# Performance work log

Measured on AMD Instinct MI355X. Metric: run time of the kernel, lower is better.

Reference implementation:

```python
import jax, jax.numpy as jnp
import numpy as np

D_MODEL = 1024
N_HEADS = 16
HEAD_DIM = D_MODEL // N_HEADS
B, S = 4, 2048


def setup_inputs() -> dict:
    key = jax.random.key(0)
    ks = jax.random.split(key, 12)
    s = 0.02
    q_input = jax.random.normal(ks[0], (B, S, D_MODEL), jnp.float32)
    k_input = jax.random.normal(ks[1], (B, S, D_MODEL), jnp.float32)
    v_input = jax.random.normal(ks[2], (B, S, D_MODEL), jnp.float32)
    # tail padding: keys at position >= valid_len are masked (True = pad)
    valid_len = jax.random.randint(ks[3], (B, 1), S // 2, S + 1)
    key_padding_mask = jnp.arange(S)[None, :] >= valid_len  # [B, S] bool
    Wq = jax.random.normal(ks[4], (D_MODEL, D_MODEL), jnp.float32) * s
    Wk = jax.random.normal(ks[5], (D_MODEL, D_MODEL), jnp.float32) * s
    Wv = jax.random.normal(ks[6], (D_MODEL, D_MODEL), jnp.float32) * s
    Wo = jax.random.normal(ks[7], (D_MODEL, D_MODEL), jnp.float32) * s
    bq = jnp.zeros((D_MODEL,), jnp.float32)
    bk = jnp.zeros((D_MODEL,), jnp.float32)
    bv = jnp.zeros((D_MODEL,), jnp.float32)
    bo = jnp.zeros((D_MODEL,), jnp.float32)
    return dict(q_input=q_input, k_input=k_input, v_input=v_input,
                key_padding_mask=key_padding_mask,
                Wq=Wq, bq=bq, Wk=Wk, bk=bk, Wv=Wv, bv=bv, Wo=Wo, bo=bo)


def reference(q_input, k_input, v_input, key_padding_mask, Wq, bq, Wk, bk, Wv, bv, Wo, bo):
    b, sq, d = q_input.shape
    sk = k_input.shape[1]
    Q = q_input @ Wq + bq
    K = k_input @ Wk + bk
    V = v_input @ Wv + bv
    # [B, H, S, Dh]
    Qh = Q.reshape(b, sq, N_HEADS, HEAD_DIM).transpose(0, 2, 1, 3)
    Kh = K.reshape(b, sk, N_HEADS, HEAD_DIM).transpose(0, 2, 1, 3)
    Vh = V.reshape(b, sk, N_HEADS, HEAD_DIM).transpose(0, 2, 1, 3)
    scores = jnp.einsum('bhqd,bhkd->bhqk', Qh, Kh) / jnp.sqrt(jnp.float32(HEAD_DIM))
    # causal mask (use_mask=True): triu(ones, diagonal=1)
    causal = jnp.triu(jnp.ones((sq, sk), bool), k=1)[None, None]
    scores = jnp.where(causal, -jnp.inf, scores)
    # key padding mask [B,1,1,Sk]
    scores = jnp.where(key_padding_mask[:, None, None, :], -jnp.inf, scores)
    all_inf = jnp.all(jnp.isinf(scores))
    probs = jax.nn.softmax(scores, axis=-1)
    probs = jnp.where(all_inf, jnp.float32(1.0) / sk, probs)
    # dropout(p=0.1) is identity in eval mode
    out = jnp.einsum('bhqk,bhkd->bhqd', probs, Vh)
    out = out.transpose(0, 2, 1, 3).reshape(b, sq, d)
    return out @ Wo + bo
```

## Files before the change

### kernel.cpp

```cpp
#include <hip/hip_runtime.h>

typedef unsigned short u16;
typedef unsigned int u32;
typedef u16 u16x8 __attribute__((ext_vector_type(8)));
typedef u16 u16x4v __attribute__((ext_vector_type(4)));
typedef u32 u32x2 __attribute__((ext_vector_type(2)));
typedef u32 u32x4 __attribute__((ext_vector_type(4)));
typedef __bf16 bf16x8 __attribute__((ext_vector_type(8)));
typedef float f32x4 __attribute__((ext_vector_type(4)));
typedef float f32x16 __attribute__((ext_vector_type(16)));

__device__ __forceinline__ u16 f2bf(float f) {
  unsigned u = __builtin_bit_cast(unsigned, f);
  u += 0x7FFF + ((u >> 16) & 1);
  return (u16)(u >> 16);
}

__device__ __forceinline__ float fast_exp2(float x) {
  return __builtin_amdgcn_exp2f(x);
}

__device__ __forceinline__ f32x4 mfma16(u16x8 a, u16x8 b, f32x4 c) {
  return __builtin_amdgcn_mfma_f32_16x16x32_bf16(
      __builtin_bit_cast(bf16x8, a), __builtin_bit_cast(bf16x8, b), c, 0, 0, 0);
}

__device__ __forceinline__ f32x16 mfma32(u16x8 a, u16x8 b, f32x16 c) {
  return __builtin_amdgcn_mfma_f32_32x32x16_bf16(
      __builtin_bit_cast(bf16x8, a), __builtin_bit_cast(bf16x8, b), c, 0, 0, 0);
}

__device__ __forceinline__ u32 cvt_pk_bf16(float lo, float hi) {
  u32 r;
  asm("v_cvt_pk_bf16_f32 %0, %1, %2" : "=v"(r) : "v"(lo), "v"(hi));
  return r;
}

constexpr int DM   = 1024;
constexpr int GK   = 1024;
constexpr int SEQ  = 2048;
constexpr int NB   = 4;
constexpr int NH   = 16;
constexpr int BK   = 64;
constexpr int LSTR = 72;

__global__ void transpose_cast_kernel(const float* __restrict__ W, u16* __restrict__ Wt) {
  __shared__ float tile[32][33];
  const int tx = threadIdx.x;
  const int ty = threadIdx.y;
  const int n0 = blockIdx.x * 32;
  const int k0 = blockIdx.y * 32;
#pragma unroll
  for (int i = 0; i < 4; ++i)
    tile[ty + i * 8][tx] = W[(size_t)(k0 + ty + i * 8) * DM + n0 + tx];
  __syncthreads();
#pragma unroll
  for (int i = 0; i < 4; ++i)
    Wt[(size_t)(n0 + ty + i * 8) * DM + k0 + tx] = f2bf(tile[tx][ty + i * 8]);
}

__global__ void vlen_kernel(const int* __restrict__ mask, int* __restrict__ vlen) {
  const int b = blockIdx.x;
  const int t = threadIdx.x;
  __shared__ int cnt[256];
  int c = 0;
  for (int s = t; s < SEQ; s += 256) c += (mask[b * SEQ + s] == 0) ? 1 : 0;
  cnt[t] = c;
  __syncthreads();
  for (int off = 128; off > 0; off >>= 1) {
    if (t < off) cnt[t] += cnt[t + off];
    __syncthreads();
  }
  if (t == 0) vlen[b] = cnt[0];
}

template <bool A_FP32>
__global__ __launch_bounds__(256) void gemm_kernel(const void* __restrict__ Av,
                                                   const u16* __restrict__ Bt,
                                                   const float* __restrict__ bias,
                                                   void* __restrict__ outv,
                                                   int out_mode) {
  __shared__ __align__(16) u16 lds_a[128 * LSTR];
  __shared__ __align__(16) u16 lds_b[128 * LSTR];
  const int tid  = threadIdx.x;
  const int lane = tid & 63;
  const int w    = tid >> 6;
  const int wm   = (w >> 1) * 64;
  const int wn   = (w & 1) * 64;
  const int lrow = lane & 15;
  const int lk   = (lane >> 4) * 8;
  const int n0   = blockIdx.x * 128;
  const int m0   = blockIdx.y * 128;

  f32x4 acc[4][4] = {};

  for (int kt = 0; kt < GK; kt += BK) {
    __syncthreads();
    if (A_FP32) {
      const float* A = (const float*)Av;
#pragma unroll
      for (int i = 0; i < 8; ++i) {
        int idx = tid + i * 256;
        int row = idx >> 4, q = idx & 15;
        float4 v = *(const float4*)(A + (size_t)(m0 + row) * GK + kt + q * 4);
        u16x4v hv = {f2bf(v.x), f2bf(v.y), f2bf(v.z), f2bf(v.w)};
        *(u16x4v*)(&lds_a[row * LSTR + q * 4]) = hv;
      }
    } else {
      const u16* A = (const u16*)Av;
#pragma unroll
      for (int i = 0; i < 4; ++i) {
        int idx = tid + i * 256;
        int row = idx >> 3, q = idx & 7;
        *(u16x8*)(&lds_a[row * LSTR + q * 8]) =
            *(const u16x8*)(A + (size_t)(m0 + row) * GK + kt + q * 8);
      }
    }
#pragma unroll
    for (int i = 0; i < 4; ++i) {
      int idx = tid + i * 256;
      int row = idx >> 3, q = idx & 7;
      *(u16x8*)(&lds_b[row * LSTR + q * 8]) =
          *(const u16x8*)(Bt + (size_t)(n0 + row) * GK + kt + q * 8);
    }
    __syncthreads();
#pragma unroll
    for (int kk = 0; kk < BK; kk += 32) {
      u16x8 am[4], bn[4];
#pragma unroll
      for (int m = 0; m < 4; ++m)
        am[m] = *(const u16x8*)(&lds_a[(wm + m * 16 + lrow) * LSTR + kk + lk]);
#pragma unroll
      for (int n = 0; n < 4; ++n)
        bn[n] = *(const u16x8*)(&lds_b[(wn + n * 16 + lrow) * LSTR + kk + lk]);
#pragma unroll
      for (int m = 0; m < 4; ++m)
#pragma unroll
        for (int n = 0; n < 4; ++n)
          acc[m][n] = mfma16(am[m], bn[n], acc[m][n]);
    }
  }

  const int r0 = (lane >> 4) * 4;
#pragma unroll
  for (int m = 0; m < 4; ++m) {
#pragma unroll
    for (int n = 0; n < 4; ++n) {
      const int col = n0 + wn + n * 16 + lrow;
      const float bval = bias[col];
#pragma unroll
      for (int r = 0; r < 4; ++r) {
        const int row = m0 + wm + m * 16 + r0 + r;
        const float v = acc[m][n][r] + bval;
        if (out_mode == 2) {
          ((float*)outv)[(size_t)row * DM + col] = v;
        } else {
          const int bb = row >> 11, s = row & (SEQ - 1);
          const int h = col >> 6, d = col & 63;
          size_t off;
          if (out_mode == 0) off = (((size_t)(bb * NH + h)) * SEQ + s) * 64 + d;
          else               off = (((size_t)(bb * NH + h)) * 64 + d) * SEQ + s;
          ((u16*)outv)[off] = f2bf(v);
        }
      }
    }
  }
}

__global__ __launch_bounds__(256) void attn_kernel(const u16* __restrict__ Qm,
                                                   const u16* __restrict__ Km,
                                                   const u16* __restrict__ Vtm,
                                                   const int* __restrict__ vlen,
                                                   u16* __restrict__ att) {
  __shared__ __align__(16) u16 smem[8192];
  char* lds_k = (char*)smem;
  char* lds_v = (char*)smem + 8192;
  const int tid  = threadIdx.x;
  const int lane = tid & 63;
  const int w    = tid >> 6;
  const int ql   = lane & 31;
  const int hi   = lane >> 5;
  const int hi4  = hi * 4;
  const int qb   = blockIdx.x;
  const int bh   = blockIdx.y;
  const int b    = bh >> 4;
  const int h    = bh & 15;
  const int valid = vlen[b];
  const int q0   = qb * 128;
  const int q0w  = q0 + w * 32;
  const int qg   = q0w + ql;
  constexpr float SC = 0.18033688011112042f;
  const float NEGB = -1e30f;

  const u16* Qbase = Qm + ((size_t)bh * SEQ + qg) * 64 + hi * 8;
  u16x8 qf[4];
#pragma unroll
  for (int s = 0; s < 4; ++s) qf[s] = *(const u16x8*)(Qbase + s * 16);

  f32x16 acc_o[2] = {};
  float m_run = NEGB, l_run = 0.f;

  const int kb_max = min((q0 + 127) >> 6, (valid - 1) >> 6);
  const int rel_base = min(qg, valid - 1);

  const u16* Kg = Km + (size_t)bh * SEQ * 64;
  const u16* Vg = Vtm + (size_t)bh * 64 * SEQ;

  for (int kb = 0; kb <= kb_max; ++kb) {
    __syncthreads();
#pragma unroll
    for (int i = 0; i < 2; ++i) {
      const int seg = tid + i * 256;
      const int row = seg >> 3, c = seg & 7;
      const int dst = (row * 128 + c * 16) ^ ((row & 7) << 4);
      *(u16x8*)(lds_k + dst) = *(const u16x8*)(Kg + ((size_t)(kb * 64 + row)) * 64 + c * 8);
      *(u16x8*)(lds_v + dst) = *(const u16x8*)(Vg + (size_t)row * SEQ + kb * 64 + c * 8);
    }
    __syncthreads();

    if (kb * 64 > q0w + 31) continue;

    f32x16 s_acc[2] = {};
    __builtin_amdgcn_s_setprio(1);
#pragma unroll
    for (int ch = 0; ch < 2; ++ch) {
#pragma unroll
      for (int s = 0; s < 4; ++s) {
        const int krow = ch * 32 + ql;
        const int off = (krow * 128 + s * 32 + hi * 16) ^ ((krow & 7) << 4);
        u16x8 kf = *(const u16x8*)(lds_k + off);
        s_acc[ch] = mfma32(kf, qf[s], s_acc[ch]);
      }
    }
    __builtin_amdgcn_s_setprio(0);

    const int rel = rel_base - kb * 64;
    float mrow = NEGB;
#pragma unroll
    for (int ch = 0; ch < 2; ++ch)
#pragma unroll
      for (int r = 0; r < 16; ++r) {
        const int koff = ch * 32 + (r & 3) + 8 * (r >> 2) + hi4;
        float tv = s_acc[ch][r] * SC;
        tv = (koff > rel) ? NEGB : tv;
        s_acc[ch][r] = tv;
        mrow = fmaxf(mrow, tv);
      }
    mrow = fmaxf(mrow, __shfl_xor(mrow, 32));
    const float mnew = fmaxf(m_run, mrow);
    const float sc_o = fast_exp2(m_run - mnew);
    m_run = mnew;
    float rs = 0.f;
#pragma unroll
    for (int ch = 0; ch < 2; ++ch)
#pragma unroll
      for (int r = 0; r < 16; ++r) {
        const float p = fast_exp2(s_acc[ch][r] - mnew);
        s_acc[ch][r] = p;
        rs += p;
      }
    rs += __shfl_xor(rs, 32);
    l_run = l_run * sc_o + rs;
#pragma unroll
    for (int dc = 0; dc < 2; ++dc)
#pragma unroll
      for (int r = 0; r < 16; ++r) acc_o[dc][r] *= sc_o;

    u16x8 pa[4];
#pragma unroll
    for (int ch = 0; ch < 2; ++ch) {
#pragma unroll
      for (int half = 0; half < 2; ++half) {
        const int pb = half * 8;
        u32 x0 = cvt_pk_bf16(s_acc[ch][pb + 0], s_acc[ch][pb + 1]);
        u32 x1 = cvt_pk_bf16(s_acc[ch][pb + 2], s_acc[ch][pb + 3]);
        u32 y0 = cvt_pk_bf16(s_acc[ch][pb + 4], s_acc[ch][pb + 5]);
        u32 y1 = cvt_pk_bf16(s_acc[ch][pb + 6], s_acc[ch][pb + 7]);
        u32x2 r0 = __builtin_amdgcn_permlane32_swap(x0, y0, false, false);
        u32x2 r1 = __builtin_amdgcn_permlane32_swap(x1, y1, false, false);
        u32x4 wds = {r0[0], r1[0], r0[1], r1[1]};
        pa[ch * 2 + half] = __builtin_bit_cast(u16x8, wds);
      }
    }

    __builtin_amdgcn_s_setprio(1);
#pragma unroll
    for (int dc = 0; dc < 2; ++dc) {
#pragma unroll
      for (int ks = 0; ks < 4; ++ks) {
        const int drow = dc * 32 + ql;
        const int off = (drow * 128 + ks * 32 + hi * 16) ^ ((drow & 7) << 4);
        u16x8 vf = *(const u16x8*)(lds_v + off);
        acc_o[dc] = mfma32(vf, pa[ks], acc_o[dc]);
      }
    }
    __builtin_amdgcn_s_setprio(0);
  }

  __syncthreads();
  const float inv_l = 1.f / l_run;
  char* wbase = (char*)smem + w * 4096;
#pragma unroll
  for (int dc = 0; dc < 2; ++dc)
#pragma unroll
    for (int rg = 0; rg < 4; ++rg) {
      u32 lo  = cvt_pk_bf16(acc_o[dc][rg * 4 + 0] * inv_l, acc_o[dc][rg * 4 + 1] * inv_l);
      u32 hiw = cvt_pk_bf16(acc_o[dc][rg * 4 + 2] * inv_l, acc_o[dc][rg * 4 + 3] * inv_l);
      const int dbase = dc * 32 + rg * 8 + hi4;
      const int off = (ql * 128 + dbase * 2) ^ ((ql & 7) << 4);
      u32x2 pr = {lo, hiw};
      *(u32x2*)(wbase + off) = pr;
    }
  __syncthreads();
  u16* attb = att + ((size_t)b * SEQ + q0) * DM + h * 64;
#pragma unroll
  for (int i = 0; i < 4; ++i) {
    const int seg = tid + i * 256;
    const int qr = seg >> 3, c = seg & 7;
    const int off = ((qr & 31) * 128 + c * 16) ^ ((qr & 7) << 4);
    u16x8 vvv = *(const u16x8*)((char*)smem + (qr >> 5) * 4096 + off);
    *(u16x8*)(attb + (size_t)qr * DM + c * 8) = vvv;
  }
}

extern "C" void kernel_launch(void* const* d_in, const int* in_sizes, int n_in,
                              void* d_out, int out_size, void* d_ws, size_t ws_size,
                              hipStream_t stream) {
  const float* q_in = (const float*)d_in[0];
  const float* k_in = (const float*)d_in[1];
  const float* v_in = (const float*)d_in[2];
  const int*   kpm  = (const int*)d_in[3];
  const float* Wq   = (const float*)d_in[4];
  const float* bq   = (const float*)d_in[5];
  const float* Wk   = (const float*)d_in[6];
  const float* bk   = (const float*)d_in[7];
  const float* Wv   = (const float*)d_in[8];
  const float* bv   = (const float*)d_in[9];
  const float* Wo   = (const float*)d_in[10];
  const float* bo   = (const float*)d_in[11];

  char* ws = (char*)d_ws;
  const size_t WSZ = (size_t)1 << 21;
  const size_t TSZ = (size_t)1 << 24;
  u16* wq_t = (u16*)(ws);
  u16* wk_t = (u16*)(ws + WSZ);
  u16* wv_t = (u16*)(ws + 2 * WSZ);
  u16* wo_t = (u16*)(ws + 3 * WSZ);
  u16* Qm   = (u16*)(ws + 4 * WSZ);
  u16* Km   = (u16*)(ws + 4 * WSZ + TSZ);
  u16* Vtm  = (u16*)(ws + 4 * WSZ + 2 * TSZ);
  u16* attb = (u16*)(ws + 4 * WSZ + 3 * TSZ);
  int* vlen = (int*)(ws + 4 * WSZ + 4 * TSZ);

  dim3 tb(32, 8), tg(32, 32);
  transpose_cast_kernel<<<tg, tb, 0, stream>>>(Wq, wq_t);
  transpose_cast_kernel<<<tg, tb, 0, stream>>>(Wk, wk_t);
  transpose_cast_kernel<<<tg, tb, 0, stream>>>(Wv, wv_t);
  transpose_cast_kernel<<<tg, tb, 0, stream>>>(Wo, wo_t);
  vlen_kernel<<<NB, 256, 0, stream>>>(kpm, vlen);

  dim3 gg(8, 64);
  gemm_kernel<true><<<gg, 256, 0, stream>>>(q_in, wq_t, bq, Qm, 0);
  gemm_kernel<true><<<gg, 256, 0, stream>>>(k_in, wk_t, bk, Km, 0);
  gemm_kernel<true><<<gg, 256, 0, stream>>>(v_in, wv_t, bv, Vtm, 1);

  attn_kernel<<<dim3(16, 64), 256, 0, stream>>>(Qm, Km, Vtm, vlen, attb);

  gemm_kernel<false><<<gg, 256, 0, stream>>>(attb, wo_t, bo, d_out, 2);
}
```

Baseline: 417.3 us.

## Pre-cast activations, use direct global-to-LDS loads, fold softmax scale, lazy rescale

```diff
diff --git a/kernel.cpp b/kernel.cpp
--- a/kernel.cpp
+++ b/kernel.cpp
@@ -3,13 +3,15 @@
 typedef unsigned short u16;
 typedef unsigned int u32;
 typedef u16 u16x8 __attribute__((ext_vector_type(8)));
-typedef u16 u16x4v __attribute__((ext_vector_type(4)));
 typedef u32 u32x2 __attribute__((ext_vector_type(2)));
 typedef u32 u32x4 __attribute__((ext_vector_type(4)));
 typedef __bf16 bf16x8 __attribute__((ext_vector_type(8)));
 typedef float f32x4 __attribute__((ext_vector_type(4)));
 typedef float f32x16 __attribute__((ext_vector_type(16)));
 
+typedef __attribute__((address_space(1))) const u32 gas_u32;
+typedef __attribute__((address_space(3))) u32 las_u32;
+
 __device__ __forceinline__ u16 f2bf(float f) {
   unsigned u = __builtin_bit_cast(unsigned, f);
   u += 0x7FFF + ((u >> 16) & 1);
@@ -34,6 +36,10 @@
   u32 r;
   asm("v_cvt_pk_bf16_f32 %0, %1, %2" : "=v"(r) : "v"(lo), "v"(hi));
   return r;
+}
+
+__device__ __forceinline__ void gload_lds16(const u16* g, u16* l) {
+  __builtin_amdgcn_global_load_lds((gas_u32*)(const void*)g, (las_u32*)(void*)l, 16, 0, 0);
 }
 
 constexpr int DM   = 1024;
@@ -41,8 +47,16 @@
 constexpr int SEQ  = 2048;
 constexpr int NB   = 4;
 constexpr int NH   = 16;
-constexpr int BK   = 64;
-constexpr int LSTR = 72;
+
+__global__ __launch_bounds__(256) void cast_bf16_kernel(const float* __restrict__ in,
+                                                        u16* __restrict__ out) {
+  const int i = blockIdx.x * 256 + threadIdx.x;
+  float4 a = ((const float4*)in)[2 * i];
+  float4 b = ((const float4*)in)[2 * i + 1];
+  u16x8 v = {f2bf(a.x), f2bf(a.y), f2bf(a.z), f2bf(a.w),
+             f2bf(b.x), f2bf(b.y), f2bf(b.z), f2bf(b.w)};
+  *(u16x8*)(out + (size_t)i * 8) = v;
+}
 
 __global__ void transpose_cast_kernel(const float* __restrict__ W, u16* __restrict__ Wt) {
   __shared__ float tile[32][33];
@@ -74,14 +88,13 @@
   if (t == 0) vlen[b] = cnt[0];
 }
 
-template <bool A_FP32>
-__global__ __launch_bounds__(256) void gemm_kernel(const void* __restrict__ Av,
+__global__ __launch_bounds__(256) void gemm_kernel(const u16* __restrict__ A,
                                                    const u16* __restrict__ Bt,
                                                    const float* __restrict__ bias,
                                                    void* __restrict__ outv,
-                                                   int out_mode) {
-  __shared__ __align__(16) u16 lds_a[128 * LSTR];
-  __shared__ __align__(16) u16 lds_b[128 * LSTR];
+                                                   int out_mode, float oscale) {
+  __shared__ __align__(16) u16 sA[128 * 64];
+  __shared__ __align__(16) u16 sB[128 * 64];
   const int tid  = threadIdx.x;
   const int lane = tid & 63;
   const int w    = tid >> 6;
@@ -92,47 +105,30 @@
   const int n0   = blockIdx.x * 128;
   const int m0   = blockIdx.y * 128;
 
+  const u16* Ab = A + (size_t)m0 * GK;
+  const u16* Bb = Bt + (size_t)n0 * GK;
+
   f32x4 acc[4][4] = {};
 
-  for (int kt = 0; kt < GK; kt += BK) {
-    __syncthreads();
-    if (A_FP32) {
-      const float* A = (const float*)Av;
-#pragma unroll
-      for (int i = 0; i < 8; ++i) {
-        int idx = tid + i * 256;
-        int row = idx >> 4, q = idx & 15;
-        float4 v = *(const float4*)(A + (size_t)(m0 + row) * GK + kt + q * 4);
-        u16x4v hv = {f2bf(v.x), f2bf(v.y), f2bf(v.z), f2bf(v.w)};
-        *(u16x4v*)(&lds_a[row * LSTR + q * 4]) = hv;
-      }
-    } else {
-      const u16* A = (const u16*)Av;
-#pragma unroll
-      for (int i = 0; i < 4; ++i) {
-        int idx = tid + i * 256;
-        int row = idx >> 3, q = idx & 7;
-        *(u16x8*)(&lds_a[row * LSTR + q * 8]) =
-            *(const u16x8*)(A + (size_t)(m0 + row) * GK + kt + q * 8);
-      }
-    }
+  for (int kt = 0; kt < GK; kt += 64) {
+    __syncthreads();
 #pragma unroll
     for (int i = 0; i < 4; ++i) {
-      int idx = tid + i * 256;
-      int row = idx >> 3, q = idx & 7;
-      *(u16x8*)(&lds_b[row * LSTR + q * 8]) =
-          *(const u16x8*)(Bt + (size_t)(n0 + row) * GK + kt + q * 8);
-    }
-    __syncthreads();
-#pragma unroll
-    for (int kk = 0; kk < BK; kk += 32) {
+      const int seg = tid + i * 256;
+      const int row = seg >> 3, c8 = (seg & 7) * 8;
+      gload_lds16(Ab + (size_t)row * GK + kt + c8, &sA[row * 64 + c8]);
+      gload_lds16(Bb + (size_t)row * GK + kt + c8, &sB[row * 64 + c8]);
+    }
+    __syncthreads();
+#pragma unroll
+    for (int kk = 0; kk < 64; kk += 32) {
       u16x8 am[4], bn[4];
 #pragma unroll
       for (int m = 0; m < 4; ++m)
-        am[m] = *(const u16x8*)(&lds_a[(wm + m * 16 + lrow) * LSTR + kk + lk]);
+        am[m] = *(const u16x8*)(&sA[(wm + m * 16 + lrow) * 64 + kk + lk]);
 #pragma unroll
       for (int n = 0; n < 4; ++n)
-        bn[n] = *(const u16x8*)(&lds_b[(wn + n * 16 + lrow) * LSTR + kk + lk]);
+        bn[n] = *(const u16x8*)(&sB[(wn + n * 16 + lrow) * 64 + kk + lk]);
 #pragma unroll
       for (int m = 0; m < 4; ++m)
 #pragma unroll
@@ -151,7 +147,7 @@
 #pragma unroll
       for (int r = 0; r < 4; ++r) {
         const int row = m0 + wm + m * 16 + r0 + r;
-        const float v = acc[m][n][r] + bval;
+        const float v = (acc[m][n][r] + bval) * oscale;
         if (out_mode == 2) {
           ((float*)outv)[(size_t)row * DM + col] = v;
         } else {
@@ -181,7 +177,7 @@
   const int ql   = lane & 31;
   const int hi   = lane >> 5;
   const int hi4  = hi * 4;
-  const int qb   = blockIdx.x;
+  const int qb   = 15 - blockIdx.x;
   const int bh   = blockIdx.y;
   const int b    = bh >> 4;
   const int h    = bh & 15;
@@ -189,7 +185,6 @@
   const int q0   = qb * 128;
   const int q0w  = q0 + w * 32;
   const int qg   = q0w + ql;
-  constexpr float SC = 0.18033688011112042f;
   const float NEGB = -1e30f;
 
   const u16* Qbase = Qm + ((size_t)bh * SEQ + qg) * 64 + hi * 8;
@@ -235,36 +230,48 @@
     __builtin_amdgcn_s_setprio(0);
 
     const int rel = rel_base - kb * 64;
+    const bool full = (kb * 64 + 63 <= q0w) && ((kb + 1) * 64 <= valid);
     float mrow = NEGB;
+    if (full) {
+#pragma unroll
+      for (int ch = 0; ch < 2; ++ch)
+#pragma unroll
+        for (int r = 0; r < 16; ++r) mrow = fmaxf(mrow, s_acc[ch][r]);
+    } else {
+#pragma unroll
+      for (int ch = 0; ch < 2; ++ch)
+#pragma unroll
+        for (int r = 0; r < 16; ++r) {
+          const int koff = ch * 32 + (r & 3) + 8 * (r >> 2) + hi4;
+          float tv = s_acc[ch][r];
+          tv = (koff > rel) ? NEGB : tv;
+          s_acc[ch][r] = tv;
+          mrow = fmaxf(mrow, tv);
+        }
+    }
+    mrow = fmaxf(mrow, __shfl_xor(mrow, 32));
+
+    if (!__all(mrow - m_run <= 8.f)) {
+      const float mnew = fmaxf(m_run, mrow);
+      const float sc_o = fast_exp2(m_run - mnew);
+      m_run = mnew;
+      l_run *= sc_o;
+#pragma unroll
+      for (int dc = 0; dc < 2; ++dc)
+#pragma unroll
+        for (int r = 0; r < 16; ++r) acc_o[dc][r] *= sc_o;
+    }
+    float rs = 0.f;
 #pragma unroll
     for (int ch = 0; ch < 2; ++ch)
 #pragma unroll
       for (int r = 0; r < 16; ++r) {
-        const int koff = ch * 32 + (r & 3) + 8 * (r >> 2) + hi4;
-        float tv = s_acc[ch][r] * SC;
-        tv = (koff > rel) ? NEGB : tv;
-        s_acc[ch][r] = tv;
-        mrow = fmaxf(mrow, tv);
-      }
-    mrow = fmaxf(mrow, __shfl_xor(mrow, 32));
-    const float mnew = fmaxf(m_run, mrow);
-    const float sc_o = fast_exp2(m_run - mnew);
-    m_run = mnew;
-    float rs = 0.f;
-#pragma unroll
-    for (int ch = 0; ch < 2; ++ch)
-#pragma unroll
-      for (int r = 0; r < 16; ++r) {
-        const float p = fast_exp2(s_acc[ch][r] - mnew);
+        const float p = fast_exp2(s_acc[ch][r] - m_run);
         s_acc[ch][r] = p;
         rs += p;
       }
     rs += __shfl_xor(rs, 32);
-    l_run = l_run * sc_o + rs;
-#pragma unroll
-    for (int dc = 0; dc < 2; ++dc)
-#pragma unroll
-      for (int r = 0; r < 16; ++r) acc_o[dc][r] *= sc_o;
+    l_run += rs;
 
     u16x8 pa[4];
 #pragma unroll
@@ -346,11 +353,16 @@
   u16* wk_t = (u16*)(ws + WSZ);
   u16* wv_t = (u16*)(ws + 2 * WSZ);
   u16* wo_t = (u16*)(ws + 3 * WSZ);
-  u16* Qm   = (u16*)(ws + 4 * WSZ);
-  u16* Km   = (u16*)(ws + 4 * WSZ + TSZ);
-  u16* Vtm  = (u16*)(ws + 4 * WSZ + 2 * TSZ);
-  u16* attb = (u16*)(ws + 4 * WSZ + 3 * TSZ);
-  int* vlen = (int*)(ws + 4 * WSZ + 4 * TSZ);
+  u16* qA   = (u16*)(ws + 4 * WSZ);
+  u16* kA   = (u16*)(ws + 4 * WSZ + TSZ);
+  u16* vA   = (u16*)(ws + 4 * WSZ + 2 * TSZ);
+  u16* Qm   = (u16*)(ws + 4 * WSZ + 3 * TSZ);
+  u16* Km   = (u16*)(ws + 4 * WSZ + 4 * TSZ);
+  u16* Vtm  = (u16*)(ws + 4 * WSZ + 5 * TSZ);
+  u16* attb = qA;
+  int* vlen = (int*)(ws + 4 * WSZ + 6 * TSZ);
+
+  const float SC = 0.18033688011112042f;
 
   dim3 tb(32, 8), tg(32, 32);
   transpose_cast_kernel<<<tg, tb, 0, stream>>>(Wq, wq_t);
@@ -359,12 +371,16 @@
   transpose_cast_kernel<<<tg, tb, 0, stream>>>(Wo, wo_t);
   vlen_kernel<<<NB, 256, 0, stream>>>(kpm, vlen);
 
+  cast_bf16_kernel<<<4096, 256, 0, stream>>>(q_in, qA);
+  cast_bf16_kernel<<<4096, 256, 0, stream>>>(k_in, kA);
+  cast_bf16_kernel<<<4096, 256, 0, stream>>>(v_in, vA);
+
   dim3 gg(8, 64);
-  gemm_kernel<true><<<gg, 256, 0, stream>>>(q_in, wq_t, bq, Qm, 0);
-  gemm_kernel<true><<<gg, 256, 0, stream>>>(k_in, wk_t, bk, Km, 0);
-  gemm_kernel<true><<<gg, 256, 0, stream>>>(v_in, wv_t, bv, Vtm, 1);
+  gemm_kernel<<<gg, 256, 0, stream>>>(qA, wq_t, bq, Qm, 0, SC);
+  gemm_kernel<<<gg, 256, 0, stream>>>(kA, wk_t, bk, Km, 0, 1.f);
+  gemm_kernel<<<gg, 256, 0, stream>>>(vA, wv_t, bv, Vtm, 1, 1.f);
 
   attn_kernel<<<dim3(16, 64), 256, 0, stream>>>(Qm, Km, Vtm, vlen, attb);
 
-  gemm_kernel<false><<<gg, 256, 0, stream>>>(attb, wo_t, bo, d_out, 2);
-}
+  gemm_kernel<<<gg, 256, 0, stream>>>(attb, wo_t, bo, d_out, 2, 1.f);
+}
```

After: 435.7 us. 4.4% more time.
